# Kernel optimization log

Hardware: AMD Instinct MI355X
Metric: run time of the kernel (lower is better)

## Reference

```python
import jax, jax.numpy as jnp
import numpy as np
import math

B, S, DIM, H = 2, 2048, 1024, 16
DH = DIM // H          # 64, per-head dim
DFF = 2048             # FCLayer hidden
NEG = -1.0e9


def setup_inputs() -> dict:
    key = jax.random.key(0)
    ks = jax.random.split(key, 10)
    glorot = jax.nn.initializers.glorot_uniform()
    de_x = jax.random.normal(ks[0], (B, S, DIM), dtype=jnp.float32)
    en_x = jax.random.normal(ks[1], (B, S, DIM), dtype=jnp.float32)
    # causal mask: 1.0 where attention is disallowed (upper triangle)
    mask = jnp.triu(jnp.ones((S, S), dtype=jnp.float32), k=1)
    # Stacked per-head projection weights for the (shared) attn_heads.
    Wq = glorot(ks[2], (H, DIM, DH), jnp.float32)
    Wk = glorot(ks[3], (H, DIM, DH), jnp.float32)
    Wv = glorot(ks[4], (H, DIM, DH), jnp.float32)
    W1 = glorot(ks[5], (DIM, DFF), jnp.float32)
    b1 = jnp.zeros((DFF,), jnp.float32)
    W2 = glorot(ks[6], (DFF, DIM), jnp.float32)
    b2 = jnp.zeros((DIM,), jnp.float32)
    return {"de_x": de_x, "en_x": en_x, "mask": mask,
            "Wq": Wq, "Wk": Wk, "Wv": Wv,
            "W1": W1, "b1": b1, "W2": W2, "b2": b2}


def _multihead(q_x, k_x, v_x, Wq, Wk, Wv, mask):
    # q_x/k_x/v_x: [B,S,DIM]; W*: [H,DIM,DH]
    q = jnp.einsum('bsd,hde->bhse', q_x, Wq)
    k = jnp.einsum('bsd,hde->bhse', k_x, Wk)
    v = jnp.einsum('bsd,hde->bhse', v_x, Wv)
    p = jnp.einsum('bhse,bhte->bhst', q, k) / math.sqrt(DH)
    if mask is not None:
        p = p + mask * NEG
    p = jax.nn.softmax(p, axis=-1)
    h = jnp.einsum('bhst,bhte->bhse', p, v)      # [B,H,S,DH]
    # concat heads along feature dim -> [B,S,DIM]
    return h.transpose(0, 2, 1, 3).reshape(q_x.shape[0], q_x.shape[1], -1)


def reference(de_x, en_x, mask, Wq, Wk, Wv, W1, b1, W2, b2):
    # Faithful to the source: compute_multihead_output ignores its attn_heads
    # arg and always uses self.attn_heads, and binds head(q=outer_en, k=outer_en,
    # v=outer_de). So:
    #   h1 = MHA(q=de_x, k=de_x, v=de_x, mask) with attn_heads weights
    #   h2 = MHA(q=en_x, k=en_x, v=h1, None)   with the SAME weights
    h1 = _multihead(de_x, de_x, de_x, Wq, Wk, Wv, mask)
    h2 = _multihead(en_x, en_x, h1, Wq, Wk, Wv, None)
    ff1 = jax.nn.relu(h2 @ W1 + b1)
    y = ff1 @ W2 + b2
    return y
```

## Files before the change

### kernel.cpp

```cpp
#include <hip/hip_runtime.h>
#include <stdint.h>


#define DEV static __device__ __forceinline__

typedef __attribute__((ext_vector_type(8))) __bf16 bf16x8;
typedef __attribute__((ext_vector_type(8))) unsigned short u16x8;
typedef __attribute__((ext_vector_type(2))) uint32_t u32x2;
typedef __attribute__((ext_vector_type(4))) float f32x4;

DEV float bf2f(uint16_t u) { union { uint32_t u; float f; } v; v.u = ((uint32_t)u) << 16; return v.f; }
DEV uint16_t f2bf(float f) {
  union { float f; uint32_t u; } v; v.f = f;
  uint32_t r = v.u + 0x7fffu + ((v.u >> 16) & 1u);
  return (uint16_t)(r >> 16);
}
DEV uint16_t f2bf_hw(float f) { return __builtin_bit_cast(unsigned short, (__bf16)f); }

DEV bf16x8 asbf(u16x8 v) { return __builtin_bit_cast(bf16x8, v); }
DEV f32x4 mfma32(bf16x8 a, bf16x8 b, f32x4 c) {
  return __builtin_amdgcn_mfma_f32_16x16x32_bf16(a, b, c, 0, 0, 0);
}

DEV void gload_lds16(const void* g, void* l) {
  __builtin_amdgcn_global_load_lds(
      (const __attribute__((address_space(1))) uint32_t*)g,
      (__attribute__((address_space(3))) uint32_t*)l, 16, 0, 0);
}

DEV int swz(int row, int slot) { return slot ^ (row & 7); }

DEV bf16x8 frag8(const uint16_t* l, int row, int slot) {
  u16x8 v = *(const u16x8*)((const char*)l + row * 128 + (swz(row, slot) << 4));
  return asbf(v);
}

__global__ void probe_k(const uint32_t* __restrict__ mask, uint32_t* __restrict__ flag) {
  flag[0] = (mask[1] & 0xFFFFu) ? 1u : 0u;
}

__global__ __launch_bounds__(256) void cvt_k(const void* __restrict__ src,
                                             uint16_t* __restrict__ dst, int n,
                                             const uint32_t* __restrict__ flag) {
  if (flag[0]) return;
  const int stride = gridDim.x * 256 * 8;
  for (int i = (blockIdx.x * 256 + threadIdx.x) * 8; i < n; i += stride) {
    const float* sf = (const float*)src + i;
    u16x8 o;
    for (int j = 0; j < 8; j++) o[j] = f2bf(sf[j]);
    *(u16x8*)(dst + i) = o;
  }
}

__global__ __launch_bounds__(256) void transpose_k(const void* __restrict__ in_,
                                                   uint16_t* __restrict__ out, int R, int C,
                                                   float scale,
                                                   const uint32_t* __restrict__ flag) {
  __shared__ uint16_t t[32][33];
  const int isbf = (int)flag[0];
  const int b = blockIdx.z;
  const float* in_f = (const float*)in_ + (size_t)b * R * C;
  const uint16_t* in_u = (const uint16_t*)in_ + (size_t)b * R * C;
  out += (size_t)b * R * C;
  const int c0 = blockIdx.x * 32, r0 = blockIdx.y * 32;
  const int tx = threadIdx.x & 31, ty = threadIdx.x >> 5;
  for (int i = 0; i < 4; i++) {
    int r = ty + i * 8;
    size_t idx = (size_t)(r0 + r) * C + c0 + tx;
    uint16_t v;
    if (isbf) v = (scale == 1.0f) ? in_u[idx] : f2bf(bf2f(in_u[idx]) * scale);
    else      v = f2bf(in_f[idx] * scale);
    t[r][tx] = v;
  }
  __syncthreads();
  for (int i = 0; i < 4; i++) {
    int r = ty + i * 8;
    out[(size_t)(c0 + r) * R + r0 + tx] = t[tx][r];
  }
}

__global__ __launch_bounds__(256) void transpose_qkv_k(const void* __restrict__ Wq,
                                                       const void* __restrict__ Wk,
                                                       const void* __restrict__ Wv,
                                                       uint16_t* __restrict__ out,
                                                       const uint32_t* __restrict__ flag) {
  __shared__ uint16_t t[32][33];
  const int isbf = (int)flag[0];
  const int which = blockIdx.z >> 4, hh = blockIdx.z & 15;
  const void* in_ = (which == 0 ? Wq : which == 1 ? Wk : Wv);
  const float scale = (which == 0) ? 0.180336880f : 1.0f;
  const int R = 1024, C = 64;
  const float* in_f = (const float*)in_ + (size_t)hh * R * C;
  const uint16_t* in_u = (const uint16_t*)in_ + (size_t)hh * R * C;
  out += ((size_t)which * 16 + hh) * R * C;
  const int c0 = blockIdx.x * 32, r0 = blockIdx.y * 32;
  const int tx = threadIdx.x & 31, ty = threadIdx.x >> 5;
  for (int i = 0; i < 4; i++) {
    int r = ty + i * 8;
    size_t idx = (size_t)(r0 + r) * C + c0 + tx;
    uint16_t v;
    if (isbf) v = (scale == 1.0f) ? in_u[idx] : f2bf(bf2f(in_u[idx]) * scale);
    else      v = f2bf(in_f[idx] * scale);
    t[r][tx] = v;
  }
  __syncthreads();
  for (int i = 0; i < 4; i++) {
    int r = ty + i * 8;
    out[(size_t)(c0 + r) * R + r0 + tx] = t[tx][r];
  }
}

__global__ __launch_bounds__(256) void proj_k(
    const uint16_t* __restrict__ Aqk_c, const void* __restrict__ Aqk_r,
    const uint16_t* __restrict__ Av_c, const void* __restrict__ Av_r,
    const uint16_t* __restrict__ Wt,
    uint16_t* __restrict__ Q, uint16_t* __restrict__ K, uint16_t* __restrict__ Vt,
    const uint32_t* __restrict__ flag) {
  __shared__ __attribute__((aligned(16))) uint16_t lA[2][128 * 64];
  __shared__ __attribute__((aligned(16))) uint16_t lB[2][128 * 64];
  const int isbf = (int)flag[0];
  const uint16_t* Aqk = isbf ? (const uint16_t*)Aqk_r : Aqk_c;
  const uint16_t* Av  = isbf ? (const uint16_t*)Av_r  : Av_c;
  const int tid = threadIdx.x, lane = tid & 63, wave = tid >> 6;
  const int g = lane >> 4;
  const int m0 = blockIdx.x * 128, n0 = blockIdx.y * 128;
  const int proj = n0 >> 10;
  const uint16_t* A = (proj == 2 ? Av : Aqk);
  const uint16_t* Bt = Wt + (size_t)n0 * 1024;
  const int wm = wave >> 1, wn = wave & 1;
  f32x4 acc[4][4] = {};
  u16x8 ra[4], rb[4];
  const int row0 = tid >> 3, slot0 = tid & 7;
  auto loadT = [&](int kt) {
    for (int i = 0; i < 4; i++) {
      int row = row0 + i * 32;
      ra[i] = *(const u16x8*)(A + (size_t)(m0 + row) * 1024 + kt + slot0 * 8);
      rb[i] = *(const u16x8*)(Bt + (size_t)row * 1024 + kt + slot0 * 8);
    }
  };
  auto writeT = [&](int buf) {
    for (int i = 0; i < 4; i++) {
      int row = row0 + i * 32;
      *(u16x8*)&lA[buf][(row * 8 + swz(row, slot0)) * 8] = ra[i];
      *(u16x8*)&lB[buf][(row * 8 + swz(row, slot0)) * 8] = rb[i];
    }
  };
  loadT(0);
  writeT(0);
  int cur = 0;
  for (int it = 0; it < 16; it++) {
    const int more = (it < 15);
    if (more) loadT((it + 1) * 64);
    __syncthreads();
    for (int kk = 0; kk < 2; kk++) {
      bf16x8 af[4], bfr[4];
      for (int fm = 0; fm < 4; fm++) af[fm] = frag8(lA[cur], wm * 64 + fm * 16 + (lane & 15), kk * 4 + g);
      for (int fn = 0; fn < 4; fn++) bfr[fn] = frag8(lB[cur], wn * 64 + fn * 16 + (lane & 15), kk * 4 + g);
      for (int fm = 0; fm < 4; fm++)
        for (int fn = 0; fn < 4; fn++)
          acc[fm][fn] = mfma32(af[fm], bfr[fn], acc[fm][fn]);
    }
    if (more) writeT(cur ^ 1);
    cur ^= 1;
  }
  if (proj != 2) {
    uint16_t* outp = (proj == 0 ? Q : K);
    for (int fm = 0; fm < 4; fm++)
      for (int fn = 0; fn < 4; fn++)
        for (int r = 0; r < 4; r++) {
          int row = m0 + wm * 64 + fm * 16 + g * 4 + r;
          int b = row >> 11, s = row & 2047;
          int col = n0 + wn * 64 + fn * 16 + (lane & 15);
          int h = (col >> 6) & 15, e = col & 63;
          outp[(((size_t)(b * 16 + h)) * 2048 + s) * 64 + e] = f2bf(acc[fm][fn][r]);
        }
  } else {
    __syncthreads();
    uint16_t* tv = (uint16_t*)lA;
    for (int fm = 0; fm < 4; fm++)
      for (int fn = 0; fn < 4; fn++)
        for (int r = 0; r < 4; r++) {
          int rl = wm * 64 + fm * 16 + g * 4 + r;
          int cl = wn * 64 + fn * 16 + (lane & 15);
          int byte = rl * 2;
          *(uint16_t*)((char*)tv + cl * 256 + ((((byte >> 4)) ^ (cl & 15)) << 4) + (byte & 15)) =
              f2bf(acc[fm][fn][r]);
        }
    __syncthreads();
    const int b = m0 >> 11, s0 = m0 & 2047;
    const int c = tid >> 1, half = tid & 1;
    const int col = n0 + c;
    const int h = (col >> 6) & 15, e = col & 63;
    uint16_t* dst = Vt + (((size_t)(b * 16 + h)) * 64 + e) * 2048 + s0 + half * 64;
    for (int j = 0; j < 8; j++) {
      int rl = half * 64 + j * 8;
      u16x8 v = *(const u16x8*)((const char*)tv + c * 256 + (((rl >> 3) ^ (c & 15)) << 4));
      *(u16x8*)(dst + j * 8) = v;
    }
  }
}

template <int CAUSAL>
__global__ __launch_bounds__(256) void attn_k(const uint16_t* __restrict__ Q,
                                              const uint16_t* __restrict__ K,
                                              const uint16_t* __restrict__ Vt,
                                              uint16_t* __restrict__ Op0,
                                              uint16_t* __restrict__ Op1,
                                              float* __restrict__ lbuf) {
  __shared__ __attribute__((aligned(16))) uint16_t lK[2][64 * 64];
  __shared__ __attribute__((aligned(16))) uint16_t lV[2][64 * 64];
  __shared__ __attribute__((aligned(16))) uint16_t lP[4][16 * 64];
  const int tid = threadIdx.x, lane = tid & 63, wave = tid >> 6;
  const int g = lane >> 4;
  const int bx = blockIdx.x, h = blockIdx.y, b = blockIdx.z;
  int qt, split, kt0, kt1;
  if (CAUSAL) {
    if (bx < 32) {
      qt = 31 - (bx >> 1);
      split = bx & 1;
      int n0 = (qt + 1) >> 1;
      kt0 = split ? n0 : 0;
      kt1 = split ? (qt + 1) : n0;
    } else {
      qt = 47 - bx; split = 0; kt0 = 0; kt1 = qt + 1;
    }
  } else {
    qt = bx & 31; split = bx >> 5; kt0 = split * 16; kt1 = kt0 + 16;
  }
  const size_t bh = (size_t)(b * 16 + h);
  const uint16_t* Qg = Q + bh * 2048 * 64;
  const uint16_t* Kg = K + bh * 2048 * 64;
  const uint16_t* Vg = Vt + bh * 64 * 2048;
  uint16_t* lPw = lP[wave];
  bf16x8 ones;
  for (int j = 0; j < 8; j++) ones[j] = (__bf16)1.0f;
  const int lrow = lane >> 3, sl = lane & 7;
  auto STAGE = [&](int buf, int kt) {
    for (int i = 0; i < 2; i++) {
      int cb = (i * 4 + wave) * 64;
      int row = (cb >> 3) + lrow;
      int so = swz(row, sl) << 3;
      gload_lds16(Kg + (size_t)(kt * 64 + row) * 64 + so, &lK[buf][cb * 8]);
      gload_lds16(Vg + (size_t)row * 2048 + kt * 64 + so, &lV[buf][cb * 8]);
    }
  };
  const int q0 = qt * 64;
  bf16x8 qf[2];
  {
    int row = q0 + wave * 16 + (lane & 15);
    for (int kk = 0; kk < 2; kk++)
      qf[kk] = asbf(*(const u16x8*)(Qg + (size_t)row * 64 + kk * 32 + g * 8));
  }
  f32x4 oacc[4] = {};
  f32x4 acc_l = {};
  const int qrow = lane & 15;
  STAGE(0, kt0);
  int buf = 0;
  for (int kt = kt0; kt < kt1; kt++) {
    __syncthreads();
    if (kt + 1 < kt1) STAGE(buf ^ 1, kt + 1);
    f32x4 s[4] = {};
    for (int kk = 0; kk < 2; kk++)
      for (int nf = 0; nf < 4; nf++)
        s[nf] = mfma32(frag8(lK[buf], nf * 16 + (lane & 15), kk * 4 + g), qf[kk], s[nf]);
    if (CAUSAL && kt == qt) {
      for (int nf = 0; nf < 4; nf++)
        for (int r = 0; r < 4; r++) {
          int kloc = nf * 16 + g * 4 + r;
          if (kloc > wave * 16 + qrow) s[nf][r] = -1e9f;
        }
    }
    for (int nf = 0; nf < 4; nf++) {
      float p0 = __builtin_amdgcn_exp2f(s[nf][0]);
      float p1 = __builtin_amdgcn_exp2f(s[nf][1]);
      float p2 = __builtin_amdgcn_exp2f(s[nf][2]);
      float p3 = __builtin_amdgcn_exp2f(s[nf][3]);
      u32x2 w;
      w[0] = ((uint32_t)f2bf_hw(p1) << 16) | f2bf_hw(p0);
      w[1] = ((uint32_t)f2bf_hw(p3) << 16) | f2bf_hw(p2);
      int slot = 2 * nf + (g >> 1);
      *(u32x2*)((char*)lPw + qrow * 128 + ((slot ^ (qrow & 7)) << 4) + ((g & 1) << 3)) = w;
    }
    for (int kk = 0; kk < 2; kk++) {
      bf16x8 pa = frag8(lPw, qrow, kk * 4 + g);
      acc_l = mfma32(pa, ones, acc_l);
      for (int df = 0; df < 4; df++)
        oacc[df] = mfma32(pa, frag8(lV[buf], df * 16 + (lane & 15), kk * 4 + g), oacc[df]);
    }
    buf ^= 1;
  }
  uint16_t* Op = split ? Op1 : Op0;
  for (int df = 0; df < 4; df++)
    for (int r = 0; r < 4; r++) {
      int srow = q0 + wave * 16 + g * 4 + r;
      int e = df * 16 + (lane & 15);
      Op[((size_t)b * 2048 + srow) * 1024 + h * 64 + e] = f2bf(oacc[df][r]);
    }
  if ((lane & 15) == 0) {
    for (int r = 0; r < 4; r++) {
      int srow = q0 + wave * 16 + g * 4 + r;
      lbuf[((size_t)(split * 2 + b) * 16 + h) * 2048 + srow] = acc_l[r];
    }
  }
}

template <int CAUSAL>
__global__ __launch_bounds__(256) void merge_k(const uint16_t* __restrict__ O0,
                                               const uint16_t* __restrict__ O1,
                                               const float* __restrict__ lbuf,
                                               uint16_t* __restrict__ out) {
  int i = (blockIdx.x * 256 + threadIdx.x) * 8;
  int sg = i >> 10;
  int b = sg >> 11, s = sg & 2047;
  int h = (i & 1023) >> 6;
  size_t i0 = ((size_t)b * 16 + h) * 2048 + s;
  size_t i1 = ((size_t)(2 + b) * 16 + h) * 2048 + s;
  float l0 = lbuf[i0];
  u16x8 o0 = *(const u16x8*)(O0 + i);
  bool two = CAUSAL ? ((s >> 6) >= 16) : true;
  u16x8 o;
  if (two) {
    float inv = 1.f / (l0 + lbuf[i1]);
    u16x8 o1v = *(const u16x8*)(O1 + i);
    for (int j = 0; j < 8; j++)
      o[j] = f2bf((bf2f(o0[j]) + bf2f(o1v[j])) * inv);
  } else {
    float inv = 1.f / l0;
    for (int j = 0; j < 8; j++) o[j] = f2bf(bf2f(o0[j]) * inv);
  }
  *(u16x8*)(out + i) = o;
}

template <int RELU>
__global__ __launch_bounds__(256) void ff_k(const uint16_t* __restrict__ A,
                                            const uint16_t* __restrict__ Bt,
                                            const void* __restrict__ bias,
                                            uint16_t* __restrict__ C, int Kdim, int N,
                                            const uint32_t* __restrict__ flag) {
  __shared__ __attribute__((aligned(16))) uint16_t lA[2][128 * 64];
  __shared__ __attribute__((aligned(16))) uint16_t lB[2][128 * 64];
  const int isbf = (int)flag[0];
  const int tid = threadIdx.x, lane = tid & 63, wave = tid >> 6;
  const int g = lane >> 4;
  const int m0 = blockIdx.x * 128, n0 = blockIdx.y * 128;
  const int wm = wave >> 1, wn = wave & 1;
  f32x4 acc[4][4] = {};
  u16x8 ra[4], rb[4];
  const int row0 = tid >> 3, slot0 = tid & 7;
  auto loadT = [&](int kt) {
    for (int i = 0; i < 4; i++) {
      int row = row0 + i * 32;
      ra[i] = *(const u16x8*)(A + (size_t)(m0 + row) * Kdim + kt + slot0 * 8);
      rb[i] = *(const u16x8*)(Bt + (size_t)(n0 + row) * Kdim + kt + slot0 * 8);
    }
  };
  auto writeT = [&](int buf) {
    for (int i = 0; i < 4; i++) {
      int row = row0 + i * 32;
      *(u16x8*)&lA[buf][(row * 8 + swz(row, slot0)) * 8] = ra[i];
      *(u16x8*)&lB[buf][(row * 8 + swz(row, slot0)) * 8] = rb[i];
    }
  };
  loadT(0);
  writeT(0);
  int cur = 0;
  const int nit = Kdim >> 6;
  for (int it = 0; it < nit; it++) {
    const int more = (it < nit - 1);
    if (more) loadT((it + 1) * 64);
    __syncthreads();
    for (int kk = 0; kk < 2; kk++) {
      bf16x8 af[4], bfr[4];
      for (int fm = 0; fm < 4; fm++) af[fm] = frag8(lA[cur], wm * 64 + fm * 16 + (lane & 15), kk * 4 + g);
      for (int fn = 0; fn < 4; fn++) bfr[fn] = frag8(lB[cur], wn * 64 + fn * 16 + (lane & 15), kk * 4 + g);
      for (int fm = 0; fm < 4; fm++)
        for (int fn = 0; fn < 4; fn++)
          acc[fm][fn] = mfma32(af[fm], bfr[fn], acc[fm][fn]);
    }
    if (more) writeT(cur ^ 1);
    cur ^= 1;
  }
  for (int fm = 0; fm < 4; fm++)
    for (int fn = 0; fn < 4; fn++) {
      int col = n0 + wn * 64 + fn * 16 + (lane & 15);
      float bv = isbf ? bf2f(((const uint16_t*)bias)[col]) : ((const float*)bias)[col];
      for (int r = 0; r < 4; r++) {
        int row = m0 + wm * 64 + fm * 16 + g * 4 + r;
        float v = acc[fm][fn][r] + bv;
        if (RELU) v = fmaxf(v, 0.f);
        C[(size_t)row * N + col] = f2bf(v);
      }
    }
}

__global__ __launch_bounds__(256) void store_k(const uint16_t* __restrict__ yb,
                                               void* __restrict__ out, int n,
                                               const uint32_t* __restrict__ flag) {
  const int isbf = (int)flag[0];
  const int stride = gridDim.x * 256 * 8;
  for (int i = (blockIdx.x * 256 + threadIdx.x) * 8; i < n; i += stride) {
    u16x8 v = *(const u16x8*)(yb + i);
    if (isbf) {
      *(u16x8*)((uint16_t*)out + i) = v;
    } else {
      float* of = (float*)out + i;
      for (int j = 0; j < 8; j++) of[j] = bf2f(v[j]);
    }
  }
}

extern "C" void kernel_launch(void* const* d_in, const int* in_sizes, int n_in,
                              void* d_out, int out_size, void* d_ws, size_t ws_size,
                              hipStream_t stream) {
  const void* de_x = d_in[0];
  const void* en_x = d_in[1];
  const void* mask = d_in[2];
  const void* Wq = d_in[3];
  const void* Wk = d_in[4];
  const void* Wv = d_in[5];
  const void* W1 = d_in[6];
  const void* b1 = d_in[7];
  const void* W2 = d_in[8];
  const void* b2 = d_in[9];

  uint16_t* ws = (uint16_t*)d_ws;
  const size_t M1 = (size_t)1 << 20;
  uint32_t* flag = (uint32_t*)ws;
  float* lbuf = (float*)(ws + 8192);
  uint16_t* Wtq = ws + 1 * M1;
  uint16_t* W1t = ws + 4 * M1;
  uint16_t* W2t = ws + 6 * M1;
  uint16_t* de_c = ws + 8 * M1;
  uint16_t* en_c = ws + 12 * M1;
  uint16_t* Qb  = ws + 16 * M1;
  uint16_t* Kb  = ws + 20 * M1;
  uint16_t* Vtb = ws + 24 * M1;
  uint16_t* h1  = ws + 28 * M1;
  uint16_t* h2  = ws + 32 * M1;
  uint16_t* ff1 = Qb;
  uint16_t* yb  = Vtb;
  uint16_t* Op0 = de_c;
  uint16_t* Op1a = h2;
  uint16_t* Op1b = h1;

  const int NX = 2 * 2048 * 1024;
  dim3 blk(256);

  probe_k<<<1, 1, 0, stream>>>((const uint32_t*)mask, flag);
  cvt_k<<<2048, blk, 0, stream>>>(de_x, de_c, NX, flag);
  cvt_k<<<2048, blk, 0, stream>>>(en_x, en_c, NX, flag);
  transpose_qkv_k<<<dim3(2, 32, 48), blk, 0, stream>>>(Wq, Wk, Wv, Wtq, flag);
  transpose_k<<<dim3(64, 32, 1), blk, 0, stream>>>(W1, W1t, 1024, 2048, 1.0f, flag);
  transpose_k<<<dim3(32, 64, 1), blk, 0, stream>>>(W2, W2t, 2048, 1024, 1.0f, flag);
  proj_k<<<dim3(32, 24), blk, 0, stream>>>(de_c, de_x, de_c, de_x, Wtq, Qb, Kb, Vtb, flag);
  attn_k<1><<<dim3(48, 16, 2), blk, 0, stream>>>(Qb, Kb, Vtb, Op0, Op1a, lbuf);
  merge_k<1><<<2048, blk, 0, stream>>>(Op0, Op1a, lbuf, h1);
  proj_k<<<dim3(32, 24), blk, 0, stream>>>(en_c, en_x, h1, h1, Wtq, Qb, Kb, Vtb, flag);
  attn_k<0><<<dim3(64, 16, 2), blk, 0, stream>>>(Qb, Kb, Vtb, Op0, Op1b, lbuf);
  merge_k<0><<<2048, blk, 0, stream>>>(Op0, Op1b, lbuf, h2);
  ff_k<1><<<dim3(32, 16), blk, 0, stream>>>(h2, W1t, b1, ff1, 1024, 2048, flag);
  ff_k<0><<<dim3(32, 8), blk, 0, stream>>>(ff1, W2t, b2, yb, 2048, 1024, flag);
  store_k<<<2048, blk, 0, stream>>>(yb, d_out, out_size, flag);
}
```

Baseline: 271.4 us.

## Share K/V tiles across two query groups in non-causal attention with 4-way split

Gives the non-causal attention its own kernel. Each block now processes 128 query rows (two 64-row groups) against one shared K/V tile stream, which halves the K/V staging per query row. The key range is split four ways instead of two, so the grid size stays the same. A new merge kernel sums four partial outputs and their row sums, using freed workspace buffers. The cost is more partial-output traffic in the merge, shorter per-block loops that expose pipeline prologue cost, and more registers per wave.

```diff
diff --git a/kernel.cpp b/kernel.cpp
--- a/kernel.cpp
+++ b/kernel.cpp
@@ -200,13 +200,12 @@
   }
 }
 
-template <int CAUSAL>
-__global__ __launch_bounds__(256) void attn_k(const uint16_t* __restrict__ Q,
-                                              const uint16_t* __restrict__ K,
-                                              const uint16_t* __restrict__ Vt,
-                                              uint16_t* __restrict__ Op0,
-                                              uint16_t* __restrict__ Op1,
-                                              float* __restrict__ lbuf) {
+__global__ __launch_bounds__(256) void attn1_k(const uint16_t* __restrict__ Q,
+                                               const uint16_t* __restrict__ K,
+                                               const uint16_t* __restrict__ Vt,
+                                               uint16_t* __restrict__ Op0,
+                                               uint16_t* __restrict__ Op1,
+                                               float* __restrict__ lbuf) {
   __shared__ __attribute__((aligned(16))) uint16_t lK[2][64 * 64];
   __shared__ __attribute__((aligned(16))) uint16_t lV[2][64 * 64];
   __shared__ __attribute__((aligned(16))) uint16_t lP[4][16 * 64];
@@ -214,18 +213,14 @@
   const int g = lane >> 4;
   const int bx = blockIdx.x, h = blockIdx.y, b = blockIdx.z;
   int qt, split, kt0, kt1;
-  if (CAUSAL) {
-    if (bx < 32) {
-      qt = 31 - (bx >> 1);
-      split = bx & 1;
-      int n0 = (qt + 1) >> 1;
-      kt0 = split ? n0 : 0;
-      kt1 = split ? (qt + 1) : n0;
-    } else {
-      qt = 47 - bx; split = 0; kt0 = 0; kt1 = qt + 1;
-    }
+  if (bx < 32) {
+    qt = 31 - (bx >> 1);
+    split = bx & 1;
+    int n0 = (qt + 1) >> 1;
+    kt0 = split ? n0 : 0;
+    kt1 = split ? (qt + 1) : n0;
   } else {
-    qt = bx & 31; split = bx >> 5; kt0 = split * 16; kt1 = kt0 + 16;
+    qt = 47 - bx; split = 0; kt0 = 0; kt1 = qt + 1;
   }
   const size_t bh = (size_t)(b * 16 + h);
   const uint16_t* Qg = Q + bh * 2048 * 64;
@@ -262,8 +257,8 @@
     f32x4 s[4] = {};
     for (int kk = 0; kk < 2; kk++)
       for (int nf = 0; nf < 4; nf++)
-        s[nf] = mfma32(frag8(lK[buf], nf * 16 + (lane & 15), kk * 4 + g), qf[kk], s[nf]);
-    if (CAUSAL && kt == qt) {
+        s[nf] = mfma32(frag8(lK[buf], nf * 16 + qrow, kk * 4 + g), qf[kk], s[nf]);
+    if (kt == qt) {
       for (int nf = 0; nf < 4; nf++)
         for (int r = 0; r < 4; r++) {
           int kloc = nf * 16 + g * 4 + r;
@@ -285,7 +280,7 @@
       bf16x8 pa = frag8(lPw, qrow, kk * 4 + g);
       acc_l = mfma32(pa, ones, acc_l);
       for (int df = 0; df < 4; df++)
-        oacc[df] = mfma32(pa, frag8(lV[buf], df * 16 + (lane & 15), kk * 4 + g), oacc[df]);
+        oacc[df] = mfma32(pa, frag8(lV[buf], df * 16 + qrow, kk * 4 + g), oacc[df]);
     }
     buf ^= 1;
   }
@@ -293,10 +288,10 @@
   for (int df = 0; df < 4; df++)
     for (int r = 0; r < 4; r++) {
       int srow = q0 + wave * 16 + g * 4 + r;
-      int e = df * 16 + (lane & 15);
+      int e = df * 16 + qrow;
       Op[((size_t)b * 2048 + srow) * 1024 + h * 64 + e] = f2bf(oacc[df][r]);
     }
-  if ((lane & 15) == 0) {
+  if (qrow == 0) {
     for (int r = 0; r < 4; r++) {
       int srow = q0 + wave * 16 + g * 4 + r;
       lbuf[((size_t)(split * 2 + b) * 16 + h) * 2048 + srow] = acc_l[r];
@@ -304,11 +299,10 @@
   }
 }
 
-template <int CAUSAL>
-__global__ __launch_bounds__(256) void merge_k(const uint16_t* __restrict__ O0,
-                                               const uint16_t* __restrict__ O1,
-                                               const float* __restrict__ lbuf,
-                                               uint16_t* __restrict__ out) {
+__global__ __launch_bounds__(256) void merge1_k(const uint16_t* __restrict__ O0,
+                                                const uint16_t* __restrict__ O1,
+                                                const float* __restrict__ lbuf,
+                                                uint16_t* __restrict__ out) {
   int i = (blockIdx.x * 256 + threadIdx.x) * 8;
   int sg = i >> 10;
   int b = sg >> 11, s = sg & 2047;
@@ -317,7 +311,7 @@
   size_t i1 = ((size_t)(2 + b) * 16 + h) * 2048 + s;
   float l0 = lbuf[i0];
   u16x8 o0 = *(const u16x8*)(O0 + i);
-  bool two = CAUSAL ? ((s >> 6) >= 16) : true;
+  bool two = (s >> 6) >= 16;
   u16x8 o;
   if (two) {
     float inv = 1.f / (l0 + lbuf[i1]);
@@ -328,6 +322,138 @@
     float inv = 1.f / l0;
     for (int j = 0; j < 8; j++) o[j] = f2bf(bf2f(o0[j]) * inv);
   }
+  *(u16x8*)(out + i) = o;
+}
+
+__global__ __launch_bounds__(256) void attn2_k(const uint16_t* __restrict__ Q,
+                                               const uint16_t* __restrict__ K,
+                                               const uint16_t* __restrict__ Vt,
+                                               uint16_t* __restrict__ Op0,
+                                               uint16_t* __restrict__ Op1,
+                                               uint16_t* __restrict__ Op2,
+                                               uint16_t* __restrict__ Op3,
+                                               float* __restrict__ lbuf) {
+  __shared__ __attribute__((aligned(16))) uint16_t lK[2][64 * 64];
+  __shared__ __attribute__((aligned(16))) uint16_t lV[2][64 * 64];
+  __shared__ __attribute__((aligned(16))) uint16_t lP[8][16 * 64];
+  const int tid = threadIdx.x, lane = tid & 63, wave = tid >> 6;
+  const int g = lane >> 4, qrow = lane & 15;
+  const int bx = blockIdx.x, h = blockIdx.y, b = blockIdx.z;
+  const int pair = bx >> 2, split = bx & 3;
+  const int kt0 = split * 8, kt1 = kt0 + 8;
+  const int q0 = pair * 128;
+  const size_t bh = (size_t)(b * 16 + h);
+  const uint16_t* Qg = Q + bh * 2048 * 64;
+  const uint16_t* Kg = K + bh * 2048 * 64;
+  const uint16_t* Vg = Vt + bh * 64 * 2048;
+  uint16_t* lP0 = lP[wave * 2];
+  uint16_t* lP1 = lP[wave * 2 + 1];
+  bf16x8 ones;
+  for (int j = 0; j < 8; j++) ones[j] = (__bf16)1.0f;
+  const int lrow = lane >> 3, sl = lane & 7;
+  auto STAGE = [&](int buf, int kt) {
+    for (int i = 0; i < 2; i++) {
+      int cb = (i * 4 + wave) * 64;
+      int row = (cb >> 3) + lrow;
+      int so = swz(row, sl) << 3;
+      gload_lds16(Kg + (size_t)(kt * 64 + row) * 64 + so, &lK[buf][cb * 8]);
+      gload_lds16(Vg + (size_t)row * 2048 + kt * 64 + so, &lV[buf][cb * 8]);
+    }
+  };
+  bf16x8 qf[2][2];
+#pragma unroll
+  for (int grp = 0; grp < 2; grp++) {
+    int row = q0 + grp * 64 + wave * 16 + qrow;
+    for (int kk = 0; kk < 2; kk++)
+      qf[grp][kk] = asbf(*(const u16x8*)(Qg + (size_t)row * 64 + kk * 32 + g * 8));
+  }
+  f32x4 oacc[2][4] = {};
+  f32x4 acc_l[2] = {};
+  auto storeP = [&](uint16_t* lPw, f32x4 (&s)[4]) {
+#pragma unroll
+    for (int nf = 0; nf < 4; nf++) {
+      float p0 = __builtin_amdgcn_exp2f(s[nf][0]);
+      float p1 = __builtin_amdgcn_exp2f(s[nf][1]);
+      float p2 = __builtin_amdgcn_exp2f(s[nf][2]);
+      float p3 = __builtin_amdgcn_exp2f(s[nf][3]);
+      u32x2 w;
+      w[0] = ((uint32_t)f2bf_hw(p1) << 16) | f2bf_hw(p0);
+      w[1] = ((uint32_t)f2bf_hw(p3) << 16) | f2bf_hw(p2);
+      int slot = 2 * nf + (g >> 1);
+      *(u32x2*)((char*)lPw + qrow * 128 + ((slot ^ (qrow & 7)) << 4) + ((g & 1) << 3)) = w;
+    }
+  };
+  STAGE(0, kt0);
+  int buf = 0;
+  for (int kt = kt0; kt < kt1; kt++) {
+    __syncthreads();
+    if (kt + 1 < kt1) STAGE(buf ^ 1, kt + 1);
+    f32x4 s0[4] = {}, s1[4] = {};
+#pragma unroll
+    for (int kk = 0; kk < 2; kk++)
+#pragma unroll
+      for (int nf = 0; nf < 4; nf++) {
+        bf16x8 kf = frag8(lK[buf], nf * 16 + qrow, kk * 4 + g);
+        s0[nf] = mfma32(kf, qf[0][kk], s0[nf]);
+        s1[nf] = mfma32(kf, qf[1][kk], s1[nf]);
+      }
+    storeP(lP0, s0);
+    storeP(lP1, s1);
+#pragma unroll
+    for (int kk = 0; kk < 2; kk++) {
+      bf16x8 pa0 = frag8(lP0, qrow, kk * 4 + g);
+      bf16x8 pa1 = frag8(lP1, qrow, kk * 4 + g);
+      acc_l[0] = mfma32(pa0, ones, acc_l[0]);
+      acc_l[1] = mfma32(pa1, ones, acc_l[1]);
+#pragma unroll
+      for (int df = 0; df < 4; df++) {
+        bf16x8 vf = frag8(lV[buf], df * 16 + qrow, kk * 4 + g);
+        oacc[0][df] = mfma32(pa0, vf, oacc[0][df]);
+        oacc[1][df] = mfma32(pa1, vf, oacc[1][df]);
+      }
+    }
+    buf ^= 1;
+  }
+  uint16_t* Op = (split == 0) ? Op0 : (split == 1) ? Op1 : (split == 2) ? Op2 : Op3;
+#pragma unroll
+  for (int grp = 0; grp < 2; grp++)
+    for (int df = 0; df < 4; df++)
+      for (int r = 0; r < 4; r++) {
+        int srow = q0 + grp * 64 + wave * 16 + g * 4 + r;
+        int e = df * 16 + qrow;
+        Op[((size_t)b * 2048 + srow) * 1024 + h * 64 + e] = f2bf(oacc[grp][df][r]);
+      }
+  if (qrow == 0) {
+#pragma unroll
+    for (int grp = 0; grp < 2; grp++)
+      for (int r = 0; r < 4; r++) {
+        int srow = q0 + grp * 64 + wave * 16 + g * 4 + r;
+        lbuf[((size_t)(split * 2 + b) * 16 + h) * 2048 + srow] = acc_l[grp][r];
+      }
+  }
+}
+
+__global__ __launch_bounds__(256) void merge2_k(const uint16_t* __restrict__ O0,
+                                                const uint16_t* __restrict__ O1,
+                                                const uint16_t* __restrict__ O2,
+                                                const uint16_t* __restrict__ O3,
+                                                const float* __restrict__ lbuf,
+                                                uint16_t* __restrict__ out) {
+  int i = (blockIdx.x * 256 + threadIdx.x) * 8;
+  int sg = i >> 10;
+  int b = sg >> 11, s = sg & 2047;
+  int h = (i & 1023) >> 6;
+  float l = 0.f;
+  for (int sp = 0; sp < 4; sp++)
+    l += lbuf[((size_t)(sp * 2 + b) * 16 + h) * 2048 + s];
+  float inv = 1.f / l;
+  u16x8 o0 = *(const u16x8*)(O0 + i);
+  u16x8 o1 = *(const u16x8*)(O1 + i);
+  u16x8 o2 = *(const u16x8*)(O2 + i);
+  u16x8 o3 = *(const u16x8*)(O3 + i);
+  u16x8 o;
+  for (int j = 0; j < 8; j++)
+    o[j] = f2bf((bf2f(o0[j]) + bf2f(o1[j]) + bf2f(o2[j]) + bf2f(o3[j])) * inv);
   *(u16x8*)(out + i) = o;
 }
 
@@ -439,9 +565,6 @@
   uint16_t* h2  = ws + 32 * M1;
   uint16_t* ff1 = Qb;
   uint16_t* yb  = Vtb;
-  uint16_t* Op0 = de_c;
-  uint16_t* Op1a = h2;
-  uint16_t* Op1b = h1;
 
   const int NX = 2 * 2048 * 1024;
   dim3 blk(256);
@@ -453,11 +576,11 @@
   transpose_k<<<dim3(64, 32, 1), blk, 0, stream>>>(W1, W1t, 1024, 2048, 1.0f, flag);
   transpose_k<<<dim3(32, 64, 1), blk, 0, stream>>>(W2, W2t, 2048, 1024, 1.0f, flag);
   proj_k<<<dim3(32, 24), blk, 0, stream>>>(de_c, de_x, de_c, de_x, Wtq, Qb, Kb, Vtb, flag);
-  attn_k<1><<<dim3(48, 16, 2), blk, 0, stream>>>(Qb, Kb, Vtb, Op0, Op1a, lbuf);
-  merge_k<1><<<2048, blk, 0, stream>>>(Op0, Op1a, lbuf, h1);
+  attn1_k<<<dim3(48, 16, 2), blk, 0, stream>>>(Qb, Kb, Vtb, de_c, h2, lbuf);
+  merge1_k<<<2048, blk, 0, stream>>>(de_c, h2, lbuf, h1);
   proj_k<<<dim3(32, 24), blk, 0, stream>>>(en_c, en_x, h1, h1, Wtq, Qb, Kb, Vtb, flag);
-  attn_k<0><<<dim3(64, 16, 2), blk, 0, stream>>>(Qb, Kb, Vtb, Op0, Op1b, lbuf);
-  merge_k<0><<<2048, blk, 0, stream>>>(Op0, Op1b, lbuf, h2);
+  attn2_k<<<dim3(64, 16, 2), blk, 0, stream>>>(Qb, Kb, Vtb, de_c, en_c, h1, h2, lbuf);
+  merge2_k<<<2048, blk, 0, stream>>>(de_c, en_c, h1, h2, lbuf, h2);
   ff_k<1><<<dim3(32, 16), blk, 0, stream>>>(h2, W1t, b1, ff1, 1024, 2048, flag);
   ff_k<0><<<dim3(32, 8), blk, 0, stream>>>(ff1, W2t, b2, yb, 2048, 1024, flag);
   store_k<<<2048, blk, 0, stream>>>(yb, d_out, out_size, flag);
```

New measurement: 270.5 us. About the same (-0.3%).
